# Kernel tuning notes

Measured on AMD Instinct MI355X. Metric: run time of the kernel, lower is better.

## Reference

```python
import jax, jax.numpy as jnp
import numpy as np

NUM_HEADS = 12
MAX_FREQ = 10.0  # 'pixel' mode default of rotary-embedding freqs
# 9 EEG frequency bands [lower, upper] Hz (delta..gamma + composites)
BANDS = np.array([[1,4],[4,8],[8,10],[10,12],[12,30],[30,45],[1,8],[8,30],[1,45]],
                 dtype=np.float32)


def _rotate_half(t):
    # (..., D) -> pairwise rotate: (x1, x2) -> (-x2, x1)
    t2 = t.reshape(*t.shape[:-1], -1, 2)
    r = jnp.stack([-t2[..., 1], t2[..., 0]], axis=-1)
    return r.reshape(*t.shape)


def _drofe_angles(head_dim):
    # freqs_for='pixel': linspace(1, max_freq/2, d/4) * pi per axis (lower/upper bound)
    nf = head_dim // 4
    freqs = jnp.pi * jnp.linspace(1.0, MAX_FREQ / 2.0, nf)          # [nf]
    bands = jnp.asarray(BANDS)                                      # [N, 2]
    lo = bands[:, 0:1] * freqs                                      # [N, nf]
    hi = bands[:, 1:2] * freqs                                      # [N, nf]
    ang = jnp.concatenate([jnp.repeat(lo, 2, axis=-1),
                           jnp.repeat(hi, 2, axis=-1)], axis=-1)    # [N, D]
    return jnp.cos(ang), jnp.sin(ang)


def setup_inputs() -> dict:
    key = jax.random.key(0)
    k1, k2, k3, k4 = jax.random.split(key, 4)
    B, N, C = 4096, 9, 768
    x = jax.random.normal(k1, (B, N, C), jnp.float32)
    demo = jax.random.uniform(k2, (B, 2), jnp.float32)  # (age_norm, gender)
    W_qkv = jax.random.normal(k3, (C, 3 * C), jnp.float32) * 0.02
    W_proj = jax.random.normal(k4, (C, C), jnp.float32) * 0.02
    b_proj = jnp.zeros((C,), jnp.float32)
    return {"x": x, "demographic_info": demo, "W_qkv": W_qkv,
            "W_proj": W_proj, "b_proj": b_proj}


def reference(x, demographic_info, W_qkv, W_proj, b_proj):
    B, N, C = x.shape
    H = NUM_HEADS
    D = C // H
    scale = D ** (-0.5)

    qkv = (x @ W_qkv).reshape(B, N, 3, H, D).transpose(2, 0, 3, 1, 4)  # [3,B,H,N,D]
    q, k, v = qkv[0], qkv[1], qkv[2]

    # demographic-conditioned 2D rotary embedding (dRoFE):
    # rotation e^{i theta} -> age*cos(theta) + i*gender*sin(theta)
    cos, sin = _drofe_angles(D)                       # [N, D]
    age = demographic_info[:, 0][:, None, None, None]     # [B,1,1,1]
    gender = demographic_info[:, 1][:, None, None, None]
    q = age * q * cos + gender * _rotate_half(q) * sin
    k = age * k * cos + gender * _rotate_half(k) * sin

    attn = jax.nn.softmax(jnp.einsum('bhnd,bhmd->bhnm', q, k) * scale, axis=-1)
    out = jnp.einsum('bhnm,bhmd->bhnd', attn, v)
    out = out.transpose(0, 2, 1, 3).reshape(B, N, C)
    return out @ W_proj + b_proj
```

## Files before the change

### kernel.cpp

```cpp
#include <hip/hip_runtime.h>
#include <cstdint>
#include <cstddef>

typedef __bf16  bf16x8 __attribute__((ext_vector_type(8)));
typedef float   f32x4  __attribute__((ext_vector_type(4)));
typedef unsigned short u16x8 __attribute__((ext_vector_type(8)));
typedef unsigned short u16x4 __attribute__((ext_vector_type(4)));

#define B_SZ  4096
#define SEQ   9
#define CDIM  768
#define HEADS 12
#define DH    64
#define MROWS (B_SZ*SEQ)
#define NQKV  (3*CDIM)
#define NPAIR (B_SZ*HEADS)
#define PPB   28
#define GK    768
#define NTK   12
#define NT2   24

#define AS1 __attribute__((address_space(1)))
#define AS3 __attribute__((address_space(3)))

__device__ inline float b2f(unsigned short u){
  union{unsigned i; float f;} x; x.i = ((unsigned)u)<<16; return x.f;
}
__device__ inline unsigned short f2b(float f){
  unsigned x = __float_as_uint(f);
  return (unsigned short)((x + 0x7fffu + ((x>>16)&1u)) >> 16);
}

#define CONV_BLKS (MROWS*CDIM/1024)
#define TCQ_BLKS  ((CDIM/64)*(NQKV/64))
#define TCP_BLKS  ((CDIM/64)*(CDIM/64))
#define PREP_BLKS (CONV_BLKS+TCQ_BLKS+TCP_BLKS+1)

__device__ inline void tconv_tile(const float* __restrict__ in,
                                  unsigned short* __restrict__ out,
                                  int R, int C, int tr, int tc,
                                  float (*tl)[65], int tid){
  int r0 = tr*64, c0 = tc*64;
  int lr = tid >> 4, lc = (tid & 15)*4;
  #pragma unroll
  for (int p=0;p<4;++p){
    float4 v = *(const float4*)(&in[(size_t)(r0+lr+p*16)*C + c0+lc]);
    tl[lr+p*16][lc]=v.x; tl[lr+p*16][lc+1]=v.y; tl[lr+p*16][lc+2]=v.z; tl[lr+p*16][lc+3]=v.w;
  }
  __syncthreads();
  #pragma unroll
  for (int p=0;p<4;++p){
    int oc = lr+p*16;
    u16x4 o;
    o.x = f2b(tl[lc+0][oc]); o.y = f2b(tl[lc+1][oc]);
    o.z = f2b(tl[lc+2][oc]); o.w = f2b(tl[lc+3][oc]);
    *(u16x4*)(&out[(size_t)(c0+oc)*R + r0 + lc]) = o;
  }
}

__global__ __launch_bounds__(256) void k_prep(const float* __restrict__ x,
                                              unsigned short* __restrict__ xb,
                                              const float* __restrict__ Wq,
                                              unsigned short* __restrict__ Wq_t,
                                              const float* __restrict__ Wp,
                                              unsigned short* __restrict__ Wp_t,
                                              float* __restrict__ cs,
                                              float* __restrict__ sn){
  __shared__ float tl[64][65];
  int blk = blockIdx.x, tid = threadIdx.x;
  if (blk < CONV_BLKS){
    int t = blk*256 + tid;
    float4 v = ((const float4*)x)[t];
    u16x4 o; o.x=f2b(v.x); o.y=f2b(v.y); o.z=f2b(v.z); o.w=f2b(v.w);
    ((u16x4*)xb)[t] = o;
  } else if (blk < CONV_BLKS+TCQ_BLKS){
    int b2 = blk - CONV_BLKS;
    tconv_tile(Wq, Wq_t, CDIM, NQKV, b2/36, b2%36, tl, tid);
  } else if (blk < CONV_BLKS+TCQ_BLKS+TCP_BLKS){
    int b3 = blk - CONV_BLKS - TCQ_BLKS;
    tconv_tile(Wp, Wp_t, CDIM, CDIM, b3/12, b3%12, tl, tid);
  } else {
    for (int t=tid; t<SEQ*DH; t+=256){
      const float blo[9] = {1.f,4.f,8.f,10.f,12.f,30.f,1.f,8.f,1.f};
      const float bhi[9] = {4.f,8.f,10.f,12.f,30.f,45.f,8.f,30.f,45.f};
      int n = t / DH, d = t - n*DH;
      int f = (d < 32) ? (d>>1) : ((d-32)>>1);
      float freq = 3.14159265358979f * (1.0f + (4.0f/15.0f)*(float)f);
      float band = (d < 32) ? blo[n] : bhi[n];
      float ang = band * freq;
      cs[t] = cosf(ang);
      sn[t] = sinf(ang);
    }
  }
}

#define GLOAD(SRC, LDSOFF) \
  __builtin_amdgcn_global_load_lds((const AS1 void*)(SRC), \
      (AS3 void*)(smem + (LDSOFF) + (w<<10)), 16, 0, 0)

#define PHASE_MID  do{ __builtin_amdgcn_s_barrier(); \
  asm volatile("s_waitcnt lgkmcnt(0)" ::: "memory"); \
  __builtin_amdgcn_sched_barrier(0); \
  __builtin_amdgcn_s_setprio(1); }while(0)
#define PHASE_END  do{ __builtin_amdgcn_s_setprio(0); \
  __builtin_amdgcn_s_barrier(); }while(0)

#define RD_A(SLOT, H) do{ _Pragma("unroll") \
  for (int m=0;m<4;++m) aQ[m] = *(const bf16x8*)((SLOT) + aRd + ((H)*4+m)*1024); }while(0)
#define RD_B(SLOT) do{ _Pragma("unroll") \
  for (int n=0;n<4;++n) bR[n] = *(const bf16x8*)((SLOT) + bRd + n*1024); }while(0)
#define MFMA_Q(H) do{ _Pragma("unroll") \
  for (int m=0;m<4;++m){ _Pragma("unroll") \
    for (int n=0;n<4;++n) \
      acc[(H)*4+m][n] = __builtin_amdgcn_mfma_f32_16x16x32_bf16(aQ[m], bR[n], acc[(H)*4+m][n], 0,0,0); } }while(0)

#define TILE_BODY(T, DB) do{ \
  const char* aS0 = smem + (DB)*16384; \
  const char* aS1 = smem + ((DB)+1)*16384; \
  const char* bS0 = smem + 65536 + (DB)*16384; \
  const char* bS1 = smem + 65536 + ((DB)+1)*16384; \
  int u1=(T)+1; if(u1>NTK-1)u1=NTK-1; int u2=(T)+2; if(u2>NTK-1)u2=NTK-1; \
  size_t o1=(size_t)u1*64+32, o2a=(size_t)u2*64, o2b=o2a+32; \
   \
  RD_A(aS0,0); RD_B(bS0); \
  GLOAD(bSrc0+o1, 65536 + (3-(DB))*16384); \
  GLOAD(bSrc1+o1, 65536 + (3-(DB))*16384 + 8192); \
  PHASE_MID; MFMA_Q(0); PHASE_END; \
   \
  RD_A(aS0,1); \
  GLOAD(aSrc0+o2a, (DB)*16384); \
  GLOAD(aSrc1+o2a, (DB)*16384 + 8192); \
  PHASE_MID; MFMA_Q(1); PHASE_END; \
   \
  RD_A(aS1,0); RD_B(bS1); \
  GLOAD(bSrc0+o2a, 65536 + (DB)*16384); \
  GLOAD(bSrc1+o2a, 65536 + (DB)*16384 + 8192); \
  PHASE_MID; MFMA_Q(0); PHASE_END; \
   \
  RD_A(aS1,1); \
  GLOAD(aSrc0+o2b, ((DB)+1)*16384); \
  GLOAD(aSrc1+o2b, ((DB)+1)*16384 + 8192); \
  PHASE_MID; MFMA_Q(1); \
  __builtin_amdgcn_s_setprio(0); \
  asm volatile("s_waitcnt vmcnt(6)" ::: "memory"); \
  __builtin_amdgcn_s_barrier(); }while(0)

template<int WRITE_F32>
__global__ __launch_bounds__(512, 2) void k_gemm8p(const unsigned short* __restrict__ A,
                                                   const unsigned short* __restrict__ Bt,
                                                   void* __restrict__ Cout,
                                                   const float* __restrict__ bias,
                                                   int M, int N, int NTN, int NWG){
  __shared__ char smem[131072];
  int wg = blockIdx.x;
  int cpx = NWG >> 3;
  int swz = (wg & 7)*cpx + (wg >> 3);
  int bm = swz / NTN, bn = swz - bm*NTN;
  int m0 = bm << 8, n0 = bn << 8;

  int tid = threadIdx.x;
  int w = tid >> 6, lane = tid & 63;
  int r = lane & 15, g4 = lane >> 4;
  int wr = w >> 2, wc = w & 3;

  int seg = g4 ^ (((r >> 3) & 1) << 1);
  int aRd = (wr*128 + r)*64 + seg*16;
  int bRd = (wc*64  + r)*64 + seg*16;

  int srow = tid >> 2;
  int gsw  = (tid & 3) ^ (((tid >> 5) & 1) << 1);
  const unsigned short* aSrc0 = A  + (size_t)(m0 + srow)*GK + gsw*8;
  const unsigned short* aSrc1 = aSrc0 + (size_t)128*GK;
  const unsigned short* bSrc0 = Bt + (size_t)(n0 + srow)*GK + gsw*8;
  const unsigned short* bSrc1 = bSrc0 + (size_t)128*GK;

  const f32x4 fz = {0.f,0.f,0.f,0.f};
  f32x4 acc[8][4];
  #pragma unroll
  for (int mi=0;mi<8;++mi)
    #pragma unroll
    for (int ni=0;ni<4;++ni) acc[mi][ni] = fz;
  bf16x8 aQ[4], bR[4];

  GLOAD(aSrc0+ 0,     0); GLOAD(aSrc1+ 0,  8192);
  GLOAD(bSrc0+ 0, 65536); GLOAD(bSrc1+ 0, 65536+ 8192);
  GLOAD(aSrc0+32, 16384); GLOAD(aSrc1+32, 16384+8192);
  GLOAD(bSrc0+32, 65536+16384); GLOAD(bSrc1+32, 65536+16384+8192);
  GLOAD(aSrc0+64, 32768); GLOAD(aSrc1+64, 32768+8192);
  GLOAD(bSrc0+64, 65536+32768); GLOAD(bSrc1+64, 65536+32768+8192);
  GLOAD(aSrc0+96, 49152); GLOAD(aSrc1+96, 49152+8192);
  asm volatile("s_waitcnt vmcnt(6)" ::: "memory");
  __builtin_amdgcn_s_barrier();

  #pragma unroll 1
  for (int tt=0; tt<NTK; tt+=2){
    TILE_BODY(tt,   0);
    TILE_BODY(tt+1, 2);
  }
  asm volatile("s_waitcnt vmcnt(0)" ::: "memory");

  if (WRITE_F32){
    #pragma unroll
    for (int mi=0;mi<8;++mi){
      #pragma unroll
      for (int ni=0;ni<4;++ni){
        int col = n0 + wc*64 + ni*16 + r;
        float bb = bias ? bias[col] : 0.f;
        #pragma unroll
        for (int q=0;q<4;++q){
          int row = m0 + wr*128 + mi*16 + g4*4 + q;
          ((float*)Cout)[(size_t)row*N + col] = acc[mi][ni][q] + bb;
        }
      }
    }
  } else {
    #pragma unroll
    for (int mi=0;mi<8;++mi){
      #pragma unroll
      for (int q=0;q<4;++q){
        int row = m0 + wr*128 + mi*16 + g4*4 + q;
        int bb = row / 9;
        int ii = row - bb*9;
        size_t rb = (size_t)bb*HEADS;
        #pragma unroll
        for (int ni=0;ni<4;++ni){
          int col = n0 + wc*64 + ni*16 + r;
          int which = (col >= 1536) ? 2 : (col >= 768 ? 1 : 0);
          int rem = col - which*768;
          int h = rem >> 6, d = rem & 63;
          size_t idx = ((rb + h)*9 + ii)*192 + which*64 + d;
          ((unsigned short*)Cout)[idx] = f2b(acc[mi][ni][q]);
        }
      }
    }
  }
}

#define TILE2(T, SL, SP) do{ \
  const char* aS = smem + (SL)*16384; \
  const char* bS = smem + 49152 + (SL)*8192; \
  int u2=(T)+2; if(u2>NT2-1)u2=NT2-1; size_t o2=(size_t)u2*32; \
  _Pragma("unroll") for (int m=0;m<4;++m) aQ[m] = *(const bf16x8*)(aS + aRd + m*1024); \
  _Pragma("unroll") for (int n=0;n<4;++n) bR[n] = *(const bf16x8*)(bS + bRd + n*1024); \
  GLOAD(aSrc0+o2, (SP)*16384); \
  GLOAD(aSrc1+o2, (SP)*16384 + 8192); \
  GLOAD(bSrc +o2, 49152 + (SP)*8192); \
  PHASE_MID; \
  _Pragma("unroll") for (int m=0;m<4;++m){ _Pragma("unroll") for (int n=0;n<4;++n) \
    acc[m][n] = __builtin_amdgcn_mfma_f32_16x16x32_bf16(aQ[m], bR[n], acc[m][n], 0,0,0); } \
  __builtin_amdgcn_s_setprio(0); \
  asm volatile("s_waitcnt vmcnt(3)" ::: "memory"); \
  __builtin_amdgcn_s_barrier(); }while(0)

__global__ __launch_bounds__(512, 4) void k_gemm2b(const unsigned short* __restrict__ A,
                                                   const unsigned short* __restrict__ Bt,
                                                   float* __restrict__ C,
                                                   const float* __restrict__ bias,
                                                   int M, int N, int NTN, int NWG){
  __shared__ char smem[73728];
  int wg = blockIdx.x;
  int cpx = NWG >> 3;
  int swz = (wg & 7)*cpx + (wg >> 3);
  int bm = swz / NTN, bn = swz - bm*NTN;
  int m0 = bm << 8, n0 = bn << 7;

  int tid = threadIdx.x;
  int w = tid >> 6, lane = tid & 63;
  int r = lane & 15, g4 = lane >> 4;
  int wr = w >> 1, wc = w & 1;

  int seg = g4 ^ (((r >> 3) & 1) << 1);
  int aRd = (wr*64 + r)*64 + seg*16;
  int bRd = (wc*64 + r)*64 + seg*16;

  int srow = tid >> 2;
  int gsw  = (tid & 3) ^ (((tid >> 5) & 1) << 1);
  const unsigned short* aSrc0 = A  + (size_t)(m0 + srow)*GK + gsw*8;
  const unsigned short* aSrc1 = aSrc0 + (size_t)128*GK;
  const unsigned short* bSrc  = Bt + (size_t)(n0 + srow)*GK + gsw*8;

  const f32x4 fz = {0.f,0.f,0.f,0.f};
  f32x4 acc[4][4];
  #pragma unroll
  for (int m=0;m<4;++m)
    #pragma unroll
    for (int n=0;n<4;++n) acc[m][n] = fz;
  bf16x8 aQ[4], bR[4];

  GLOAD(aSrc0+ 0, 0);     GLOAD(aSrc1+ 0, 8192);       GLOAD(bSrc+ 0, 49152);
  GLOAD(aSrc0+32, 16384); GLOAD(aSrc1+32, 16384+8192); GLOAD(bSrc+32, 49152+8192);
  asm volatile("s_waitcnt vmcnt(3)" ::: "memory");
  __builtin_amdgcn_s_barrier();

  #pragma unroll 1
  for (int tt=0; tt<NT2; tt+=3){
    TILE2(tt,   0, 2);
    TILE2(tt+1, 1, 0);
    TILE2(tt+2, 2, 1);
  }
  asm volatile("s_waitcnt vmcnt(0)" ::: "memory");

  #pragma unroll
  for (int mi=0;mi<4;++mi){
    #pragma unroll
    for (int ni=0;ni<4;++ni){
      int col = n0 + wc*64 + ni*16 + r;
      float bb = bias ? bias[col] : 0.f;
      #pragma unroll
      for (int q=0;q<4;++q){
        int row = m0 + wr*64 + mi*16 + g4*4 + q;
        C[(size_t)row*N + col] = acc[mi][ni][q] + bb;
      }
    }
  }
}

__global__ __launch_bounds__(256) void k_attn(const unsigned short* __restrict__ qkv,
                                              const float* __restrict__ demo,
                                              const float* __restrict__ cs,
                                              const float* __restrict__ sn,
                                              unsigned short* __restrict__ out){
  __shared__ __align__(16) unsigned int kv[PPB][SEQ][68];
  __shared__ float s_cs[SEQ*DH], s_sn[SEQ*DH];
  int tid = threadIdx.x;
  for (int t=tid; t<SEQ*DH; t+=256){ s_cs[t]=cs[t]; s_sn[t]=sn[t]; }

  int pr = tid / 9, i = tid - pr*9;
  int pair = blockIdx.x*PPB + pr;
  bool act = (pr < PPB) && (pair < NPAIR);
  int b = 0, h = 0; float age = 0.f, gen = 0.f;
  const unsigned short* base = qkv;
  if (act){
    b = pair / HEADS; h = pair - b*HEADS;
    age = demo[2*b]; gen = demo[2*b+1];
    base = qkv + (size_t)pair*(SEQ*192);
  }
  __syncthreads();

  float qr[64];
  if (act){
    const u16x8* qp = (const u16x8*)(base + (size_t)i*192);
    const u16x8* kp = (const u16x8*)(base + (size_t)i*192 + 64);
    const uint4* vp = (const uint4*)(base + (size_t)i*192 + 128);
    #pragma unroll
    for (int t8=0;t8<8;++t8){
      u16x8 qv = qp[t8], kw = kp[t8];
      unsigned int kp4[4];
      #pragma unroll
      for (int e=0;e<8;e+=2){
        int d = t8*8+e;
        float c0=s_cs[i*64+d], s0=s_sn[i*64+d];
        float c1=s_cs[i*64+d+1], s1=s_sn[i*64+d+1];
        float q0=b2f(qv[e]), q1=b2f(qv[e+1]);
        qr[d]   = age*q0*c0 - gen*q1*s0;
        qr[d+1] = age*q1*c1 + gen*q0*s1;
        float k0=b2f(kw[e]), k1=b2f(kw[e+1]);
        float r0 = age*k0*c0 - gen*k1*s0;
        float r1 = age*k1*c1 + gen*k0*s1;
        kp4[e>>1] = (unsigned)f2b(r0) | ((unsigned)f2b(r1)<<16);
      }
      *(uint4*)(&kv[pr][i][t8*4]) = *(const uint4*)kp4;
      *(uint4*)(&kv[pr][i][32+t8*4]) = vp[t8];
    }
  }
  __syncthreads();

  if (!act) return;

  float s[9]; float mx = -1e30f;
  #pragma unroll
  for (int j=0;j<9;++j){
    const uint4* kr = (const uint4*)(&kv[pr][j][0]);
    float acc = 0.f;
    #pragma unroll
    for (int q8=0;q8<8;++q8){
      uint4 kk = kr[q8];
      acc += qr[q8*8+0]*b2f((unsigned short)(kk.x&0xffffu)) + qr[q8*8+1]*b2f((unsigned short)(kk.x>>16));
      acc += qr[q8*8+2]*b2f((unsigned short)(kk.y&0xffffu)) + qr[q8*8+3]*b2f((unsigned short)(kk.y>>16));
      acc += qr[q8*8+4]*b2f((unsigned short)(kk.z&0xffffu)) + qr[q8*8+5]*b2f((unsigned short)(kk.z>>16));
      acc += qr[q8*8+6]*b2f((unsigned short)(kk.w&0xffffu)) + qr[q8*8+7]*b2f((unsigned short)(kk.w>>16));
    }
    s[j] = acc * 0.125f;
    mx = fmaxf(mx, s[j]);
  }
  float den = 0.f;
  #pragma unroll
  for (int j=0;j<9;++j){ s[j] = __expf(s[j]-mx); den += s[j]; }
  float inv = 1.f/den;
  #pragma unroll
  for (int j=0;j<9;++j) s[j] *= inv;

  unsigned short* op = out + (size_t)(b*SEQ+i)*CDIM + h*DH;
  #pragma unroll
  for (int hf=0; hf<2; ++hf){
    float o[32];
    #pragma unroll
    for (int d=0;d<32;++d) o[d]=0.f;
    #pragma unroll
    for (int j=0;j<9;++j){
      float p = s[j];
      const uint4* vr = (const uint4*)(&kv[pr][j][32 + hf*16]);
      #pragma unroll
      for (int q4=0;q4<4;++q4){
        uint4 vv = vr[q4];
        o[q4*8+0] += p*b2f((unsigned short)(vv.x&0xffffu));
        o[q4*8+1] += p*b2f((unsigned short)(vv.x>>16));
        o[q4*8+2] += p*b2f((unsigned short)(vv.y&0xffffu));
        o[q4*8+3] += p*b2f((unsigned short)(vv.y>>16));
        o[q4*8+4] += p*b2f((unsigned short)(vv.z&0xffffu));
        o[q4*8+5] += p*b2f((unsigned short)(vv.z>>16));
        o[q4*8+6] += p*b2f((unsigned short)(vv.w&0xffffu));
        o[q4*8+7] += p*b2f((unsigned short)(vv.w>>16));
      }
    }
    #pragma unroll
    for (int t8=0;t8<4;++t8){
      u16x8 v;
      #pragma unroll
      for (int e=0;e<8;++e) v[e]=f2b(o[t8*8+e]);
      ((u16x8*)op)[hf*4 + t8] = v;
    }
  }
}

extern "C" void kernel_launch(void* const* d_in, const int* in_sizes, int n_in,
                              void* d_out, int out_size, void* d_ws, size_t ws_size,
                              hipStream_t stream){
  const float* x    = (const float*)d_in[0];
  const float* demo = (const float*)d_in[1];
  const float* Wq   = (const float*)d_in[2];
  const float* Wp   = (const float*)d_in[3];
  const float* bp   = (const float*)d_in[4];
  float* outp = (float*)d_out;

  char* wsb = (char*)d_ws;
  unsigned short* xb   = (unsigned short*)wsb;
  unsigned short* Wq_t = (unsigned short*)(wsb + 56623104);
  unsigned short* Wp_t = (unsigned short*)(wsb + 60162048);
  float* cs = (float*)(wsb + 61341696);
  float* sn = cs + SEQ*DH;
  unsigned short* qkv  = (unsigned short*)(wsb + 61346304);

  k_prep <<< PREP_BLKS, 256, 0, stream >>> (x, xb, Wq, Wq_t, Wp, Wp_t, cs, sn);

  {
    int nwg = (MROWS/256)*(NQKV/256);
    k_gemm8p<0><<< nwg, 512, 0, stream >>>
        (xb, Wq_t, qkv, nullptr, MROWS, NQKV, NQKV/256, nwg);
  }

  k_attn <<< (NPAIR + PPB - 1)/PPB, 256, 0, stream >>> (qkv, demo, cs, sn, xb);

  {
    int nwg = (MROWS/256)*(CDIM/128);
    k_gemm2b<<< nwg, 512, 0, stream >>>
        (xb, Wp_t, outp, bp, MROWS, CDIM, CDIM/128, nwg);
  }
}
```

Before: 352.2 us.

## Stage attention q/k/v tile into LDS with coalesced loads and rotated layout

The attention kernel now copies each block's whole contiguous qkv slab into shared memory with coalesced 16-byte loads. Rows are stored with a per-row rotation of 16-byte groups to avoid bank conflicts, replacing the strided per-thread global reads of q, k and v. The block shrinks to 192 threads handling 21 head-pairs, so fewer lanes sit idle. The trade-off is a larger LDS footprint per block and extra index arithmetic for the rotated addressing, which may reduce occupancy.

```diff
diff --git a/kernel.cpp b/kernel.cpp
--- a/kernel.cpp
+++ b/kernel.cpp
@@ -15,7 +15,6 @@
 #define MROWS (B_SZ*SEQ)
 #define NQKV  (3*CDIM)
 #define NPAIR (B_SZ*HEADS)
-#define PPB   28
 #define GK    768
 #define NTK   12
 #define NT2   24
@@ -315,52 +314,68 @@
   }
 }
 
-__global__ __launch_bounds__(256) void k_attn(const unsigned short* __restrict__ qkv,
+#define PPB2 21
+__global__ __launch_bounds__(192) void k_attn(const unsigned short* __restrict__ qkv,
                                               const float* __restrict__ demo,
                                               const float* __restrict__ cs,
                                               const float* __restrict__ sn,
                                               unsigned short* __restrict__ out){
-  __shared__ __align__(16) unsigned int kv[PPB][SEQ][68];
+  __shared__ __align__(16) unsigned int kvs[PPB2*SEQ*96];
   __shared__ float s_cs[SEQ*DH], s_sn[SEQ*DH];
   int tid = threadIdx.x;
-  for (int t=tid; t<SEQ*DH; t+=256){ s_cs[t]=cs[t]; s_sn[t]=sn[t]; }
+  for (int t=tid; t<SEQ*DH; t+=192){ s_cs[t]=cs[t]; s_sn[t]=sn[t]; }
+
+  int pair0 = blockIdx.x*PPB2;
+  int npairs = NPAIR - pair0; if (npairs > PPB2) npairs = PPB2;
+  int nchunk = npairs*216;
+
+  const uint4* src = (const uint4*)(qkv + (size_t)pair0*(SEQ*192));
+  for (int c = tid; c < nchunk; c += 192){
+    uint4 v = src[c];
+    int row = c/24, g = c - row*24;
+    int rm = row % 24;
+    int gp = g + rm; if (gp >= 24) gp -= 24;
+    *(uint4*)(&kvs[row*96 + gp*4]) = v;
+  }
+  __syncthreads();
 
   int pr = tid / 9, i = tid - pr*9;
-  int pair = blockIdx.x*PPB + pr;
-  bool act = (pr < PPB) && (pair < NPAIR);
+  bool act = (pr < npairs);
   int b = 0, h = 0; float age = 0.f, gen = 0.f;
-  const unsigned short* base = qkv;
   if (act){
+    int pair = pair0 + pr;
     b = pair / HEADS; h = pair - b*HEADS;
     age = demo[2*b]; gen = demo[2*b+1];
-    base = qkv + (size_t)pair*(SEQ*192);
-  }
-  __syncthreads();
+  }
 
   float qr[64];
+  int r_own = pr*9 + i;
+  int rm_own = r_own % 24;
   if (act){
-    const u16x8* qp = (const u16x8*)(base + (size_t)i*192);
-    const u16x8* kp = (const u16x8*)(base + (size_t)i*192 + 64);
-    const uint4* vp = (const uint4*)(base + (size_t)i*192 + 128);
     #pragma unroll
     for (int t8=0;t8<8;++t8){
-      u16x8 qv = qp[t8], kw = kp[t8];
-      unsigned int kp4[4];
-      #pragma unroll
-      for (int e=0;e<8;e+=2){
-        int d = t8*8+e;
+      int gq = t8 + rm_own;      if (gq >= 24) gq -= 24;
+      int gk = t8 + 8 + rm_own;  if (gk >= 24) gk -= 24;
+      uint4 qv = *(const uint4*)(&kvs[r_own*96 + gq*4]);
+      uint4 kw = *(const uint4*)(&kvs[r_own*96 + gk*4]);
+      unsigned int kp[4];
+      const unsigned int qa[4] = {qv.x, qv.y, qv.z, qv.w};
+      const unsigned int ka[4] = {kw.x, kw.y, kw.z, kw.w};
+      #pragma unroll
+      for (int p2=0;p2<4;++p2){
+        int d = t8*8 + p2*2;
         float c0=s_cs[i*64+d], s0=s_sn[i*64+d];
         float c1=s_cs[i*64+d+1], s1=s_sn[i*64+d+1];
-        float q0=b2f(qv[e]), q1=b2f(qv[e+1]);
+        float q0=b2f((unsigned short)(qa[p2]&0xffffu)), q1=b2f((unsigned short)(qa[p2]>>16));
         qr[d]   = age*q0*c0 - gen*q1*s0;
         qr[d+1] = age*q1*c1 + gen*q0*s1;
-        float k0=b2f(kw[e]), k1=b2f(kw[e+1]);
+        float k0=b2f((unsigned short)(ka[p2]&0xffffu)), k1=b2f((unsigned short)(ka[p2]>>16));
         float r0 = age*k0*c0 - gen*k1*s0;
         float r1 = age*k1*c1 + gen*k0*s1;
-        kp4[e>>1] = (unsigned)f2b(r0) | ((unsigned)f2b(r1)<<16);
-      }
-      *(uint4*)(&kv[pr][i][t8*4]) = *(const uint4*)kp4;
-      *(uint4*)(&kv[pr][i][32+t8*4]) = vp[t8];
+        kp[p2] = (unsigned)f2b(r0) | ((unsigned)f2b(r1)<<16);
+      }
+      uint4 kv4; kv4.x=kp[0]; kv4.y=kp[1]; kv4.z=kp[2]; kv4.w=kp[3];
+      *(uint4*)(&kvs[r_own*96 + gk*4]) = kv4;
     }
   }
   __syncthreads();
@@ -370,15 +385,17 @@
   float s[9]; float mx = -1e30f;
   #pragma unroll
   for (int j=0;j<9;++j){
-    const uint4* kr = (const uint4*)(&kv[pr][j][0]);
+    int rj = pr*9 + j;
+    int rmj = rj % 24;
     float acc = 0.f;
     #pragma unroll
-    for (int q8=0;q8<8;++q8){
-      uint4 kk = kr[q8];
-      acc += qr[q8*8+0]*b2f((unsigned short)(kk.x&0xffffu)) + qr[q8*8+1]*b2f((unsigned short)(kk.x>>16));
-      acc += qr[q8*8+2]*b2f((unsigned short)(kk.y&0xffffu)) + qr[q8*8+3]*b2f((unsigned short)(kk.y>>16));
-      acc += qr[q8*8+4]*b2f((unsigned short)(kk.z&0xffffu)) + qr[q8*8+5]*b2f((unsigned short)(kk.z>>16));
-      acc += qr[q8*8+6]*b2f((unsigned short)(kk.w&0xffffu)) + qr[q8*8+7]*b2f((unsigned short)(kk.w>>16));
+    for (int t8=0;t8<8;++t8){
+      int gk = t8 + 8 + rmj; if (gk >= 24) gk -= 24;
+      uint4 kk = *(const uint4*)(&kvs[rj*96 + gk*4]);
+      acc += qr[t8*8+0]*b2f((unsigned short)(kk.x&0xffffu)) + qr[t8*8+1]*b2f((unsigned short)(kk.x>>16));
+      acc += qr[t8*8+2]*b2f((unsigned short)(kk.y&0xffffu)) + qr[t8*8+3]*b2f((unsigned short)(kk.y>>16));
+      acc += qr[t8*8+4]*b2f((unsigned short)(kk.z&0xffffu)) + qr[t8*8+5]*b2f((unsigned short)(kk.z>>16));
+      acc += qr[t8*8+6]*b2f((unsigned short)(kk.w&0xffffu)) + qr[t8*8+7]*b2f((unsigned short)(kk.w>>16));
     }
     s[j] = acc * 0.125f;
     mx = fmaxf(mx, s[j]);
@@ -399,10 +416,18 @@
     #pragma unroll
     for (int j=0;j<9;++j){
       float p = s[j];
-      const uint4* vr = (const uint4*)(&kv[pr][j][32 + hf*16]);
+      int rj = pr*9 + j;
+      int rmj = rj % 24;
+      #pragma unroll
+      for (int q4=0;q4<2;++q4){
+        int gv = 16 + hf*2 + q4 + rmj; if (gv >= 24) gv -= 24;
+        (void)gv;
+      }
       #pragma unroll
       for (int q4=0;q4<4;++q4){
-        uint4 vv = vr[q4];
+        int g = 16 + hf*4 + q4;
+        int gp = g + rmj; if (gp >= 24) gp -= 24;
+        uint4 vv = *(const uint4*)(&kvs[rj*96 + gp*4]);
         o[q4*8+0] += p*b2f((unsigned short)(vv.x&0xffffu));
         o[q4*8+1] += p*b2f((unsigned short)(vv.x>>16));
         o[q4*8+2] += p*b2f((unsigned short)(vv.y&0xffffu));
@@ -449,7 +474,7 @@
         (xb, Wq_t, qkv, nullptr, MROWS, NQKV, NQKV/256, nwg);
   }
 
-  k_attn <<< (NPAIR + PPB - 1)/PPB, 256, 0, stream >>> (qkv, demo, cs, sn, xb);
+  k_attn <<< (NPAIR + PPB2 - 1)/PPB2, 192, 0, stream >>> (qkv, demo, cs, sn, xb);
 
   {
     int nwg = (MROWS/256)*(CDIM/128);
```

New measurement: 425.6 us. 20.9% more time.
